# Optimization experiments

Measured on AMD Instinct MI355X. Metric: run time of the kernel, lower is better.

## Reference

```python
import jax, jax.numpy as jnp
import numpy as np

N_EMB = 256
HEAD_SIZE = 64
B, S = 4, 4096


def setup_inputs() -> dict:
    key = jax.random.key(0)
    k1, k2, k3, k4 = jax.random.split(key, 4)
    return {
        "ini_emb": jax.random.normal(k1, (B, S, N_EMB), dtype=jnp.float32),
        "wk": jax.random.normal(k2, (N_EMB, HEAD_SIZE), dtype=jnp.float32) * (N_EMB ** -0.5),
        "wq": jax.random.normal(k3, (N_EMB, HEAD_SIZE), dtype=jnp.float32) * (N_EMB ** -0.5),
        "wv": jax.random.normal(k4, (N_EMB, HEAD_SIZE), dtype=jnp.float32) * (N_EMB ** -0.5),
    }


def reference(ini_emb, wk, wq, wv):
    # projections: [B,S,E] @ [E,H] -> [B,S,H]
    k = ini_emb @ wk
    q = ini_emb @ wq
    v = ini_emb @ wv
    # scores: [B,S,S]; NOTE: source scales by n_emb**-0.5, not head_size**-0.5
    scores = jnp.einsum("bqh,bkh->bqk", q, k) * (N_EMB ** -0.5)
    attn = jax.nn.softmax(scores, axis=-1)
    # output: [B,S,H]
    return jnp.einsum("bqk,bkh->bqh", attn, v)
```

## Files before the change

### kernel.cpp

```cpp
#include <hip/hip_runtime.h>


typedef short short4v __attribute__((ext_vector_type(4)));
typedef short short8v __attribute__((ext_vector_type(8)));
typedef float floatx4 __attribute__((ext_vector_type(4)));
typedef unsigned short u16;
typedef unsigned int u32;

#define SEQ 4096
#define EMB 256
#define HD 64
#define PADA 264

static __device__ __forceinline__ u16 f2bf(float x) {
    union { float f; unsigned u; } v; v.f = x;
    unsigned r = v.u + 0x7FFFu + ((v.u >> 16) & 1u);
    return (u16)(r >> 16);
}

static __device__ __forceinline__ short4v pack_bf4(float a, float b, float c, float d) {
    union { u32 u[2]; short4v s; } x;
    x.u[0] = (u32)f2bf(a) | ((u32)f2bf(b) << 16);
    x.u[1] = (u32)f2bf(c) | ((u32)f2bf(d) << 16);
    return x.s;
}

__global__ __launch_bounds__(256) void prep_w(
    const float* __restrict__ wk, const float* __restrict__ wq, const float* __restrict__ wv,
    u16* __restrict__ wt) {
    const int nt = blockIdx.x;
    const int t = threadIdx.x;
#pragma unroll
    for (int ss = 0; ss < 2; ++ss) {
        int slot = t + ss * 256;
        int kc = slot >> 6, lane = slot & 63;
        int ln15 = lane & 15, lq = lane >> 4;
        int cg = nt * 16 + ln15;
        int mat = cg >> 6, col = cg & 63;
        const float* W = (mat == 0) ? wq : (mat == 1) ? wk : wv;
        const float s = (mat == 0) ? 0.0625f * 1.44269504088896f : 1.0f;
        u32 w4[4];
#pragma unroll
        for (int p = 0; p < 2; ++p) {
#pragma unroll
            for (int d = 0; d < 2; ++d) {
                int e0 = kc * 32 + lq * 8 + p * 4 + d * 2;
                u16 lo = f2bf(W[(e0 + 0) * HD + col] * s);
                u16 hi = f2bf(W[(e0 + 1) * HD + col] * s);
                w4[p * 2 + d] = (u32)lo | ((u32)hi << 16);
            }
        }
        u32* dst = (u32*)wt + ((size_t)(nt * 8 + kc) * 64 + lane) * 4;
        *(uint4*)dst = make_uint4(w4[0], w4[1], w4[2], w4[3]);
    }
}

__global__ __launch_bounds__(256) void proj_mfma(
    const float* __restrict__ emb, const u16* __restrict__ wt,
    u16* __restrict__ qb, u16* __restrict__ kb, u16* __restrict__ vbt) {
    __shared__ u16 a_s[16 * PADA];
    const int t = threadIdx.x;
    const int lane = t & 63;
    const int wave = t >> 6;
    const int ln15 = lane & 15;
    const int lq = lane >> 4;
    const size_t row0 = (size_t)blockIdx.x * 16;

#pragma unroll
    for (int c = 0; c < 4; ++c) {
        int f = t + c * 256;
        int row = f >> 6, e4 = (f & 63) * 4;
        float4 v = *(const float4*)(emb + (row0 + row) * EMB + e4);
        ushort4 o;
        o.x = f2bf(v.x); o.y = f2bf(v.y); o.z = f2bf(v.z); o.w = f2bf(v.w);
        *(ushort4*)&a_s[row * PADA + e4] = o;
    }
    __syncthreads();

    floatx4 acc[3];
#pragma unroll
    for (int j = 0; j < 3; ++j) {
        floatx4 z = { 0.f, 0.f, 0.f, 0.f };
        acc[j] = z;
    }

#pragma unroll
    for (int kc = 0; kc < 8; ++kc) {
        short8v a = *(const short8v*)&a_s[ln15 * PADA + kc * 32 + lq * 8];
#pragma unroll
        for (int j = 0; j < 3; ++j) {
            short8v b = *(const short8v*)(wt + (((size_t)(wave * 3 + j) * 8 + kc) * 64 + lane) * 8);
            acc[j] = __builtin_amdgcn_mfma_f32_16x16x32_bf16(a, b, acc[j], 0, 0, 0);
        }
    }

#pragma unroll
    for (int j = 0; j < 3; ++j) {
        int cg = (wave * 3 + j) * 16 + ln15;
        int mat = cg >> 6, col = cg & 63;
        if (mat < 2) {
            u16* O = (mat == 0) ? qb : kb;
#pragma unroll
            for (int r = 0; r < 4; ++r)
                O[(row0 + lq * 4 + r) * HD + col] = f2bf(acc[j][r]);
        } else {
            ushort4 o4;
            o4.x = f2bf(acc[j][0]); o4.y = f2bf(acc[j][1]);
            o4.z = f2bf(acc[j][2]); o4.w = f2bf(acc[j][3]);
            size_t bidx = row0 >> 12;
            size_t sl = (row0 & 4095) + lq * 4;
            *(ushort4*)&vbt[(bidx * 64 + col) * SEQ + sl] = o4;
        }
    }
}

__global__ __launch_bounds__(256) void attn_kernel(
    const u16* __restrict__ qb, const u16* __restrict__ kb, const u16* __restrict__ vbt,
    float* __restrict__ po, float* __restrict__ pml) {
    __shared__ float ored[64 * 66];
    __shared__ float lred[4 * 64];

    const int t = threadIdx.x;
    const int lane = t & 63;
    const int wave = t >> 6;
    const int ln15 = lane & 15;
    const int lq = lane >> 4;

    const int part = blockIdx.x;
    const int b = part >> 8;
    const int qt = (part >> 2) & 63;
    const int split = part & 3;
    const int q0 = qt * 64;

    const u16* __restrict__ qpb = qb + ((size_t)b * SEQ + q0) * HD;
    const u16* __restrict__ kpb = kb + (size_t)b * SEQ * HD;
    const u16* __restrict__ vpb = vbt + (size_t)b * HD * SEQ;

    short8v qf[4][2];
#pragma unroll
    for (int nt = 0; nt < 4; ++nt)
#pragma unroll
        for (int h = 0; h < 2; ++h)
            qf[nt][h] = *(const short8v*)(qpb + (size_t)(nt * 16 + ln15) * HD + h * 32 + lq * 8);

    floatx4 oacc[4][4];
#pragma unroll
    for (int ht = 0; ht < 4; ++ht)
#pragma unroll
        for (int nt = 0; nt < 4; ++nt) {
            floatx4 z = { 0.f, 0.f, 0.f, 0.f };
            oacc[ht][nt] = z;
        }
    float lacc[4] = { 0.f, 0.f, 0.f, 0.f };

    for (int tt = 0; tt < 16; ++tt) {
        const int kw = (split * 16 + tt) * 64 + wave * 16;

        short8v kf0 = *(const short8v*)(kpb + (size_t)(kw + ln15) * HD + lq * 8);
        short8v kf1 = *(const short8v*)(kpb + (size_t)(kw + ln15) * HD + 32 + lq * 8);
        short4v vf[4];
#pragma unroll
        for (int ht = 0; ht < 4; ++ht)
            vf[ht] = *(const short4v*)(vpb + (size_t)(ht * 16 + ln15) * SEQ + kw + lq * 4);

        floatx4 s[4];
#pragma unroll
        for (int nt = 0; nt < 4; ++nt) {
            floatx4 z = { 0.f, 0.f, 0.f, 0.f };
            s[nt] = __builtin_amdgcn_mfma_f32_16x16x32_bf16(kf0, qf[nt][0], z, 0, 0, 0);
            s[nt] = __builtin_amdgcn_mfma_f32_16x16x32_bf16(kf1, qf[nt][1], s[nt], 0, 0, 0);
        }

        short4v pf[4];
#pragma unroll
        for (int nt = 0; nt < 4; ++nt) {
            float p0 = __builtin_amdgcn_exp2f(s[nt][0]);
            float p1 = __builtin_amdgcn_exp2f(s[nt][1]);
            float p2 = __builtin_amdgcn_exp2f(s[nt][2]);
            float p3 = __builtin_amdgcn_exp2f(s[nt][3]);
            lacc[nt] += (p0 + p1) + (p2 + p3);
            pf[nt] = pack_bf4(p0, p1, p2, p3);
        }

#pragma unroll
        for (int ht = 0; ht < 4; ++ht)
#pragma unroll
            for (int nt = 0; nt < 4; ++nt)
                oacc[ht][nt] = __builtin_amdgcn_mfma_f32_16x16x16bf16_1k(
                    vf[ht], pf[nt], oacc[ht][nt], 0, 0, 0);
    }

#pragma unroll
    for (int nt = 0; nt < 4; ++nt) {
        lacc[nt] += __shfl_xor(lacc[nt], 16);
        lacc[nt] += __shfl_xor(lacc[nt], 32);
    }
    if (lq == 0) {
#pragma unroll
        for (int nt = 0; nt < 4; ++nt)
            lred[wave * 64 + nt * 16 + ln15] = lacc[nt];
    }

    for (int s4 = 0; s4 < 4; ++s4) {
        if (wave == s4) {
#pragma unroll
            for (int ht = 0; ht < 4; ++ht)
#pragma unroll
                for (int nt = 0; nt < 4; ++nt)
#pragma unroll
                    for (int r = 0; r < 4; ++r) {
                        int idx = (ht * 16 + lq * 4 + r) * 66 + nt * 16 + ln15;
                        if (s4 == 0) ored[idx] = oacc[ht][nt][r];
                        else ored[idx] += oacc[ht][nt][r];
                    }
        }
        __syncthreads();
    }

    float* __restrict__ pob = po + (size_t)part * 4096;
#pragma unroll
    for (int i = 0; i < 16; ++i) {
        int f = t + i * 256;
        pob[f] = ored[(f >> 6) * 66 + (f & 63)];
    }
    if (t < 64)
        pml[part * 64 + t] = lred[t] + lred[64 + t] + lred[128 + t] + lred[192 + t];
}

__global__ __launch_bounds__(256) void reduce_kernel(
    const float* __restrict__ po, const float* __restrict__ pml,
    float* __restrict__ out) {
    __shared__ float os[64 * 67];
    __shared__ float ls[64];
    const int t = threadIdx.x;
    const int part0 = blockIdx.x * 4;
    const int bq = blockIdx.x;

#pragma unroll
    for (int i = 0; i < 16; ++i) {
        int f = t + i * 256;
        float a = po[(size_t)(part0 + 0) * 4096 + f] + po[(size_t)(part0 + 1) * 4096 + f]
                + po[(size_t)(part0 + 2) * 4096 + f] + po[(size_t)(part0 + 3) * 4096 + f];
        os[(f >> 6) * 67 + (f & 63)] = a;
    }
    if (t < 64)
        ls[t] = pml[(part0 + 0) * 64 + t] + pml[(part0 + 1) * 64 + t]
              + pml[(part0 + 2) * 64 + t] + pml[(part0 + 3) * 64 + t];
    __syncthreads();

    const size_t orow0 = ((size_t)(bq >> 6) * SEQ + (size_t)(bq & 63) * 64);
#pragma unroll
    for (int i = 0; i < 4; ++i) {
        int f4 = t + i * 256;
        int q = f4 >> 4, h4 = (f4 & 15) * 4;
        float inv = 1.0f / ls[q];
        float4 r;
        r.x = os[(h4 + 0) * 67 + q] * inv;
        r.y = os[(h4 + 1) * 67 + q] * inv;
        r.z = os[(h4 + 2) * 67 + q] * inv;
        r.w = os[(h4 + 3) * 67 + q] * inv;
        *(float4*)&out[(orow0 + q) * HD + h4] = r;
    }
}

extern "C" void kernel_launch(void* const* d_in, const int* in_sizes, int n_in,
                              void* d_out, int out_size, void* d_ws, size_t ws_size,
                              hipStream_t stream) {
    const float* emb = (const float*)d_in[0];
    const float* wk  = (const float*)d_in[1];
    const float* wq  = (const float*)d_in[2];
    const float* wv  = (const float*)d_in[3];

    u16* qb  = (u16*)d_ws;
    u16* kb  = (u16*)((char*)d_ws + (size_t)2 * 1024 * 1024);
    u16* vbt = (u16*)((char*)d_ws + (size_t)4 * 1024 * 1024);
    u16* wt  = (u16*)((char*)d_ws + (size_t)6 * 1024 * 1024);
    float* po  = (float*)((char*)d_ws + (size_t)6 * 1024 * 1024 + 256 * 1024);
    float* pml = (float*)((char*)d_ws + (size_t)22 * 1024 * 1024 + 256 * 1024);
    float* out = (float*)d_out;

    prep_w<<<12, 256, 0, stream>>>(wk, wq, wv, wt);
    proj_mfma<<<1024, 256, 0, stream>>>(emb, wt, qb, kb, vbt);
    attn_kernel<<<1024, 256, 0, stream>>>(qb, kb, vbt, po, pml);
    reduce_kernel<<<256, 256, 0, stream>>>(po, pml, out);
}
```

Measured before the change: 138.5 us.

## Prefetch next K/V tile, stage Q in LDS, cheaper bf16 pack, finer reduce grid

The attention loop now loads the next K and V fragments before computing on the current tile, so global-load latency can overlap the MFMA work. Q fragments are staged once in padded shared memory and reread each iteration instead of being held in registers, which frees VGPRs for the prefetch buffers. The bf16 packing of the probabilities switches to a single perm instruction with round-half-up bias instead of round-to-nearest-even. The reduce kernel is split into four times as many blocks, each handling 16 query rows. The prefetch reads one tile past the end on the last iteration (unused data), and the extra LDS traffic for Q may offset the register savings.

Measured after the change: 140.5 us. No clear change (+1.5%).

```diff
diff --git a/kernel.cpp b/kernel.cpp
--- a/kernel.cpp
+++ b/kernel.cpp
@@ -11,6 +11,7 @@
 #define EMB 256
 #define HD 64
 #define PADA 264
+#define PADQ 68
 
 static __device__ __forceinline__ u16 f2bf(float x) {
     union { float f; unsigned u; } v; v.f = x;
@@ -18,11 +19,10 @@
     return (u16)(r >> 16);
 }
 
-static __device__ __forceinline__ short4v pack_bf4(float a, float b, float c, float d) {
-    union { u32 u[2]; short4v s; } x;
-    x.u[0] = (u32)f2bf(a) | ((u32)f2bf(b) << 16);
-    x.u[1] = (u32)f2bf(c) | ((u32)f2bf(d) << 16);
-    return x.s;
+static __device__ __forceinline__ u32 pack_rn(float lo, float hi) {
+    union { float f; u32 u; } a, b;
+    a.f = lo; b.f = hi;
+    return __builtin_amdgcn_perm(b.u + 0x8000u, a.u + 0x8000u, 0x07060302u);
 }
 
 __global__ __launch_bounds__(256) void prep_w(
@@ -117,6 +117,7 @@
 __global__ __launch_bounds__(256) void attn_kernel(
     const u16* __restrict__ qb, const u16* __restrict__ kb, const u16* __restrict__ vbt,
     float* __restrict__ po, float* __restrict__ pml) {
+    __shared__ u16 q_s[64 * PADQ];
     __shared__ float ored[64 * 66];
     __shared__ float lred[4 * 64];
 
@@ -136,12 +137,13 @@
     const u16* __restrict__ kpb = kb + (size_t)b * SEQ * HD;
     const u16* __restrict__ vpb = vbt + (size_t)b * HD * SEQ;
 
-    short8v qf[4][2];
-#pragma unroll
-    for (int nt = 0; nt < 4; ++nt)
-#pragma unroll
-        for (int h = 0; h < 2; ++h)
-            qf[nt][h] = *(const short8v*)(qpb + (size_t)(nt * 16 + ln15) * HD + h * 32 + lq * 8);
+#pragma unroll
+    for (int c = 0; c < 4; ++c) {
+        int f = t + c * 256;
+        int row = f >> 4, h4 = (f & 15) * 4;
+        *(ushort4*)&q_s[row * PADQ + h4] = *(const ushort4*)(qpb + (size_t)row * HD + h4);
+    }
+    __syncthreads();
 
     floatx4 oacc[4][4];
 #pragma unroll
@@ -153,22 +155,31 @@
         }
     float lacc[4] = { 0.f, 0.f, 0.f, 0.f };
 
+    int kw = split * 16 * 64 + wave * 16;
+    short8v kf0 = *(const short8v*)(kpb + (size_t)(kw + ln15) * HD + lq * 8);
+    short8v kf1 = *(const short8v*)(kpb + (size_t)(kw + ln15) * HD + 32 + lq * 8);
+    short4v vf[4];
+#pragma unroll
+    for (int ht = 0; ht < 4; ++ht)
+        vf[ht] = *(const short4v*)(vpb + (size_t)(ht * 16 + ln15) * SEQ + kw + lq * 4);
+
     for (int tt = 0; tt < 16; ++tt) {
-        const int kw = (split * 16 + tt) * 64 + wave * 16;
-
-        short8v kf0 = *(const short8v*)(kpb + (size_t)(kw + ln15) * HD + lq * 8);
-        short8v kf1 = *(const short8v*)(kpb + (size_t)(kw + ln15) * HD + 32 + lq * 8);
-        short4v vf[4];
+        const int kwn = kw + 64;
+        short8v nk0 = *(const short8v*)(kpb + (size_t)(kwn + ln15) * HD + lq * 8);
+        short8v nk1 = *(const short8v*)(kpb + (size_t)(kwn + ln15) * HD + 32 + lq * 8);
+        short4v nv[4];
 #pragma unroll
         for (int ht = 0; ht < 4; ++ht)
-            vf[ht] = *(const short4v*)(vpb + (size_t)(ht * 16 + ln15) * SEQ + kw + lq * 4);
+            nv[ht] = *(const short4v*)(vpb + (size_t)(ht * 16 + ln15) * SEQ + kwn + lq * 4);
 
         floatx4 s[4];
 #pragma unroll
         for (int nt = 0; nt < 4; ++nt) {
+            short8v q0f = *(const short8v*)&q_s[(nt * 16 + ln15) * PADQ + lq * 8];
+            short8v q1f = *(const short8v*)&q_s[(nt * 16 + ln15) * PADQ + 32 + lq * 8];
             floatx4 z = { 0.f, 0.f, 0.f, 0.f };
-            s[nt] = __builtin_amdgcn_mfma_f32_16x16x32_bf16(kf0, qf[nt][0], z, 0, 0, 0);
-            s[nt] = __builtin_amdgcn_mfma_f32_16x16x32_bf16(kf1, qf[nt][1], s[nt], 0, 0, 0);
+            s[nt] = __builtin_amdgcn_mfma_f32_16x16x32_bf16(kf0, q0f, z, 0, 0, 0);
+            s[nt] = __builtin_amdgcn_mfma_f32_16x16x32_bf16(kf1, q1f, s[nt], 0, 0, 0);
         }
 
         short4v pf[4];
@@ -179,7 +190,10 @@
             float p2 = __builtin_amdgcn_exp2f(s[nt][2]);
             float p3 = __builtin_amdgcn_exp2f(s[nt][3]);
             lacc[nt] += (p0 + p1) + (p2 + p3);
-            pf[nt] = pack_bf4(p0, p1, p2, p3);
+            union { u32 u[2]; short4v s4; } pk;
+            pk.u[0] = pack_rn(p0, p1);
+            pk.u[1] = pack_rn(p2, p3);
+            pf[nt] = pk.s4;
         }
 
 #pragma unroll
@@ -188,6 +202,11 @@
             for (int nt = 0; nt < 4; ++nt)
                 oacc[ht][nt] = __builtin_amdgcn_mfma_f32_16x16x16bf16_1k(
                     vf[ht], pf[nt], oacc[ht][nt], 0, 0, 0);
+
+        kw = kwn;
+        kf0 = nk0; kf1 = nk1;
+#pragma unroll
+        for (int ht = 0; ht < 4; ++ht) vf[ht] = nv[ht];
     }
 
 #pragma unroll
@@ -230,37 +249,36 @@
 __global__ __launch_bounds__(256) void reduce_kernel(
     const float* __restrict__ po, const float* __restrict__ pml,
     float* __restrict__ out) {
-    __shared__ float os[64 * 67];
-    __shared__ float ls[64];
+    __shared__ float os[16 * 65];
+    __shared__ float ls[16];
     const int t = threadIdx.x;
-    const int part0 = blockIdx.x * 4;
-    const int bq = blockIdx.x;
-
-#pragma unroll
-    for (int i = 0; i < 16; ++i) {
+    const int bq = blockIdx.x >> 2;
+    const int sub = blockIdx.x & 3;
+    const int part0 = bq * 4;
+    const int q0l = sub * 16;
+
+#pragma unroll
+    for (int i = 0; i < 4; ++i) {
         int f = t + i * 256;
-        float a = po[(size_t)(part0 + 0) * 4096 + f] + po[(size_t)(part0 + 1) * 4096 + f]
-                + po[(size_t)(part0 + 2) * 4096 + f] + po[(size_t)(part0 + 3) * 4096 + f];
-        os[(f >> 6) * 67 + (f & 63)] = a;
-    }
-    if (t < 64)
-        ls[t] = pml[(part0 + 0) * 64 + t] + pml[(part0 + 1) * 64 + t]
-              + pml[(part0 + 2) * 64 + t] + pml[(part0 + 3) * 64 + t];
+        int h = f >> 4, q = f & 15;
+        size_t base = (size_t)part0 * 4096 + h * 64 + q0l + q;
+        float a = po[base] + po[base + 4096] + po[base + 8192] + po[base + 12288];
+        os[q * 65 + h] = a;
+    }
+    if (t < 16)
+        ls[t] = pml[part0 * 64 + q0l + t] + pml[(part0 + 1) * 64 + q0l + t]
+              + pml[(part0 + 2) * 64 + q0l + t] + pml[(part0 + 3) * 64 + q0l + t];
     __syncthreads();
 
-    const size_t orow0 = ((size_t)(bq >> 6) * SEQ + (size_t)(bq & 63) * 64);
-#pragma unroll
-    for (int i = 0; i < 4; ++i) {
-        int f4 = t + i * 256;
-        int q = f4 >> 4, h4 = (f4 & 15) * 4;
-        float inv = 1.0f / ls[q];
-        float4 r;
-        r.x = os[(h4 + 0) * 67 + q] * inv;
-        r.y = os[(h4 + 1) * 67 + q] * inv;
-        r.z = os[(h4 + 2) * 67 + q] * inv;
-        r.w = os[(h4 + 3) * 67 + q] * inv;
-        *(float4*)&out[(orow0 + q) * HD + h4] = r;
-    }
+    const int q = t >> 4, h4 = (t & 15) * 4;
+    const float inv = 1.0f / ls[q];
+    float4 r;
+    r.x = os[q * 65 + h4 + 0] * inv;
+    r.y = os[q * 65 + h4 + 1] * inv;
+    r.z = os[q * 65 + h4 + 2] * inv;
+    r.w = os[q * 65 + h4 + 3] * inv;
+    size_t orow = (size_t)(bq >> 6) * SEQ + (size_t)(bq & 63) * 64 + q0l + q;
+    *(float4*)&out[orow * HD + h4] = r;
 }
 
 extern "C" void kernel_launch(void* const* d_in, const int* in_sizes, int n_in,
@@ -282,5 +300,5 @@
     prep_w<<<12, 256, 0, stream>>>(wk, wq, wv, wt);
     proj_mfma<<<1024, 256, 0, stream>>>(emb, wt, qb, kb, vbt);
     attn_kernel<<<1024, 256, 0, stream>>>(qb, kb, vbt, po, pml);
-    reduce_kernel<<<256, 256, 0, stream>>>(po, pml, out);
-}
+    reduce_kernel<<<1024, 256, 0, stream>>>(po, pml, out);
+}
```
